# Kernel tuning notes

Hardware: AMD Instinct MI355X
Metric: run time of the kernel (lower is better)

## Reference

```python
import jax, jax.numpy as jnp
import numpy as np

HIDDEN = 768
VOCAB = 32000
HS1 = 128


def setup_inputs() -> dict:
    key = jax.random.key(0)
    k_tk, k_hs, k_w1, k_b1, k_w2, k_b2 = jax.random.split(key, 6)
    B, S = 16, 4096
    tk = jax.random.randint(k_tk, (B, S), 0, VOCAB, dtype=jnp.int64)
    hs0 = jax.random.normal(k_hs, (B, S, HIDDEN), dtype=jnp.float32)
    # lin1: in_features = VOCAB + HIDDEN, out = HS1.  Stored as [in, out]
    # (transpose of torch's [out, in]); rows [0:VOCAB] multiply the one-hot,
    # rows [VOCAB:] multiply hs0, matching cat([one_hot, hs0], -1).
    bound1 = 1.0 / np.sqrt(VOCAB + HIDDEN)
    W1 = jax.random.uniform(k_w1, (VOCAB + HIDDEN, HS1), jnp.float32, -bound1, bound1)
    b1 = jax.random.uniform(k_b1, (HS1,), jnp.float32, -bound1, bound1)
    bound2 = 1.0 / np.sqrt(HS1)
    W2 = jax.random.uniform(k_w2, (HS1, 1), jnp.float32, -bound2, bound2)
    b2 = jax.random.uniform(k_b2, (1,), jnp.float32, -bound2, bound2)
    return {"tk": tk, "hs0": hs0, "W1": W1, "b1": b1, "W2": W2, "b2": b2}


def reference(tk, hs0, W1, b1, W2, b2):
    # one_hot(tk) @ W1[:VOCAB] is exactly a row gather (entries are 0/1),
    # so compute it as a gather fused with the hs0 projection.
    tok_part = W1[:VOCAB][tk]                      # [B, S, HS1] gather
    hs_part = jnp.einsum("bsh,hk->bsk", hs0, W1[VOCAB:])  # [B, S, HS1]
    h = jax.nn.relu(tok_part + hs_part + b1)       # [B, S, HS1]
    out = jnp.einsum("bsk,ko->bso", h, W2) + b2    # [B, S, 1]
    return out.squeeze(-1)                         # [B, S]
```

## Files before the change

### kernel.cpp

```cpp
#include <hip/hip_runtime.h>

#define HIDDEN 768
#define VOCAB  32000
#define HS1    128
#define KSTEPS (HIDDEN / 32)

typedef __attribute__((ext_vector_type(8))) short bf16x8;
typedef __attribute__((ext_vector_type(4))) float f32x4;

__device__ __forceinline__ unsigned short f2bf(float f) {
    union { float f; unsigned u; } x; x.f = f;
    unsigned r = x.u + 0x7fffu + ((x.u >> 16) & 1u);
    return (unsigned short)(r >> 16);
}

__global__ void pack_b_kernel(const float* __restrict__ W1,
                              unsigned short* __restrict__ Bp) {
    int idx  = blockIdx.x * 256 + threadIdx.x;
    int j    = idx & 7;
    int lane = (idx >> 3) & 63;
    int nt   = (idx >> 9) & 7;
    int ks   = idx >> 12;
    int k = ks * 32 + (lane >> 4) * 8 + j;
    int n = nt * 16 + (lane & 15);
    float v = W1[(size_t)(VOCAB + k) * HS1 + n];
    Bp[idx] = f2bf(v);
}

__launch_bounds__(256, 2)
__global__ void classifier_kernel(const int* __restrict__ tk,
                                  const float* __restrict__ hs0,
                                  const float* __restrict__ W1,
                                  const float* __restrict__ b1,
                                  const float* __restrict__ W2,
                                  const float* __restrict__ b2,
                                  const unsigned short* __restrict__ Bp,
                                  float* __restrict__ out) {
    const int lane = threadIdx.x & 63;
    const int wave = threadIdx.x >> 6;
    const int quad = lane >> 4;
    const int col  = lane & 15;
    const int row0 = (blockIdx.x * 4 + wave) * 32;

    const float* pa0 = hs0 + (size_t)(row0 + col) * HIDDEN + quad * 8;
    const float* pa1 = pa0 + (size_t)16 * HIDDEN;
    const unsigned short* pb0 = Bp + lane * 8;

    int toks[8];
#pragma unroll
    for (int mt = 0; mt < 2; ++mt)
#pragma unroll
        for (int reg = 0; reg < 4; ++reg)
            toks[mt * 4 + reg] = tk[row0 + mt * 16 + quad * 4 + reg];

    f32x4 acc[2][8];
#pragma unroll
    for (int mt = 0; mt < 2; ++mt)
#pragma unroll
        for (int nt = 0; nt < 8; ++nt)
            acc[mt][nt] = (f32x4){0.f, 0.f, 0.f, 0.f};

    struct Frag {
        f32x4 a0l, a0h, a1l, a1h;
        bf16x8 b[8];
    };

    auto load_frag = [&](int ks) {
        Frag f;
        const f32x4* x0 = (const f32x4*)(pa0 + ks * 32);
        const f32x4* x1 = (const f32x4*)(pa1 + ks * 32);
        f.a0l = __builtin_nontemporal_load(x0);
        f.a0h = __builtin_nontemporal_load(x0 + 1);
        f.a1l = __builtin_nontemporal_load(x1);
        f.a1h = __builtin_nontemporal_load(x1 + 1);
        const unsigned short* pb  = pb0 + ks * 4096;
        const unsigned short* pb2 = pb + 2048;
#pragma unroll
        for (int nt = 0; nt < 4; ++nt) {
            f.b[nt]     = *(const bf16x8*)(pb  + nt * 512);
            f.b[nt + 4] = *(const bf16x8*)(pb2 + nt * 512);
        }
        return f;
    };

    auto cvt8 = [&](f32x4 lo, f32x4 hi) {
        bf16x8 r;
        r[0] = (short)f2bf(lo[0]); r[1] = (short)f2bf(lo[1]);
        r[2] = (short)f2bf(lo[2]); r[3] = (short)f2bf(lo[3]);
        r[4] = (short)f2bf(hi[0]); r[5] = (short)f2bf(hi[1]);
        r[6] = (short)f2bf(hi[2]); r[7] = (short)f2bf(hi[3]);
        return r;
    };

    auto compute = [&](const Frag& f) {
        bf16x8 af0 = cvt8(f.a0l, f.a0h);
        bf16x8 af1 = cvt8(f.a1l, f.a1h);
#pragma unroll
        for (int nt = 0; nt < 8; ++nt) {
            acc[0][nt] = __builtin_amdgcn_mfma_f32_16x16x32_bf16(af0, f.b[nt], acc[0][nt], 0, 0, 0);
            acc[1][nt] = __builtin_amdgcn_mfma_f32_16x16x32_bf16(af1, f.b[nt], acc[1][nt], 0, 0, 0);
        }
    };

    Frag f0 = load_frag(0);
    Frag f1 = load_frag(1);
    Frag f2 = load_frag(2);
#pragma unroll 1
    for (int ks = 3; ks < KSTEPS; ks += 3) {
        compute(f0); f0 = load_frag(ks);
        compute(f1); f1 = load_frag(ks + 1);
        compute(f2); f2 = load_frag(ks + 2);
    }
    compute(f0);
    compute(f1);
    compute(f2);

    const float bb2 = b2[0];
    float b1v[8], w2v[8];
#pragma unroll
    for (int nt = 0; nt < 8; ++nt) {
        b1v[nt] = b1[nt * 16 + col];
        w2v[nt] = W2[nt * 16 + col];
    }
#pragma unroll
    for (int mt = 0; mt < 2; ++mt) {
#pragma unroll
        for (int reg = 0; reg < 4; ++reg) {
            int r = row0 + mt * 16 + quad * 4 + reg;
            const float* wrow = W1 + (size_t)toks[mt * 4 + reg] * HS1;
            float p = 0.f;
#pragma unroll
            for (int nt = 0; nt < 8; ++nt) {
                float v = acc[mt][nt][reg] + wrow[nt * 16 + col] + b1v[nt];
                v = fmaxf(v, 0.f);
                p = fmaf(v, w2v[nt], p);
            }
            p += __shfl_xor(p, 1);
            p += __shfl_xor(p, 2);
            p += __shfl_xor(p, 4);
            p += __shfl_xor(p, 8);
            if (col == 0) out[r] = p + bb2;
        }
    }
}

extern "C" void kernel_launch(void* const* d_in, const int* in_sizes, int n_in,
                              void* d_out, int out_size, void* d_ws, size_t ws_size,
                              hipStream_t stream) {
    const int*   tk  = (const int*)d_in[0];
    const float* hs0 = (const float*)d_in[1];
    const float* W1  = (const float*)d_in[2];
    const float* b1  = (const float*)d_in[3];
    const float* W2  = (const float*)d_in[4];
    const float* b2  = (const float*)d_in[5];
    float* out = (float*)d_out;
    unsigned short* Bp = (unsigned short*)d_ws;

    pack_b_kernel<<<(HIDDEN * HS1) / 256, 256, 0, stream>>>(W1, Bp);

    int n_tokens = in_sizes[0];
    int grid = n_tokens / 128;
    classifier_kernel<<<grid, 256, 0, stream>>>(tk, hs0, W1, b1, W2, b2, Bp, out);
}
```

Before: 304.4 us.

## Stage hs0 tiles through per-wave LDS with coalesced loads and double buffering

Global reads of hs0 are reorganised so each wave loads full 128-byte row segments (8 lanes per row) into a padded per-wave LDS buffer, then reads MFMA A-fragments from LDS. This replaces the earlier strided per-lane fragment loads, with the aim of better coalescing, and double-buffers LDS with a one-stage register prefetch of global data and B fragments. The pack kernel is also changed to read W1 contiguously and scatter the writes. The risks are added LDS traffic, no explicit barrier (it relies on intra-wave ordering), and a shallower prefetch depth than the previous three-stage register pipeline.

```diff
diff --git a/kernel.cpp b/kernel.cpp
--- a/kernel.cpp
+++ b/kernel.cpp
@@ -3,7 +3,8 @@
 #define HIDDEN 768
 #define VOCAB  32000
 #define HS1    128
-#define KSTEPS (HIDDEN / 32)
+#define NSTAGE 24
+#define LSTRIDE 36
 
 typedef __attribute__((ext_vector_type(8))) short bf16x8;
 typedef __attribute__((ext_vector_type(4))) float f32x4;
@@ -16,15 +17,15 @@
 
 __global__ void pack_b_kernel(const float* __restrict__ W1,
                               unsigned short* __restrict__ Bp) {
-    int idx  = blockIdx.x * 256 + threadIdx.x;
-    int j    = idx & 7;
-    int lane = (idx >> 3) & 63;
-    int nt   = (idx >> 9) & 7;
-    int ks   = idx >> 12;
-    int k = ks * 32 + (lane >> 4) * 8 + j;
-    int n = nt * 16 + (lane & 15);
-    float v = W1[(size_t)(VOCAB + k) * HS1 + n];
-    Bp[idx] = f2bf(v);
+    int tid = blockIdx.x * 256 + threadIdx.x;
+    float v = W1[(size_t)VOCAB * HS1 + tid];
+    int k = tid >> 7;
+    int n = tid & 127;
+    int ks = k >> 5, kr = k & 31;
+    int quad = kr >> 3, j = kr & 7;
+    int nt = n >> 4, c = n & 15;
+    int lane = quad * 16 + c;
+    Bp[(((ks * 8 + nt) * 64 + lane) << 3) + j] = f2bf(v);
 }
 
 __launch_bounds__(256, 2)
@@ -36,15 +37,20 @@
                                   const float* __restrict__ b2,
                                   const unsigned short* __restrict__ Bp,
                                   float* __restrict__ out) {
+    __shared__ float lds[4][2][32 * LSTRIDE];
+
     const int lane = threadIdx.x & 63;
     const int wave = threadIdx.x >> 6;
     const int quad = lane >> 4;
     const int col  = lane & 15;
     const int row0 = (blockIdx.x * 4 + wave) * 32;
 
-    const float* pa0 = hs0 + (size_t)(row0 + col) * HIDDEN + quad * 8;
-    const float* pa1 = pa0 + (size_t)16 * HIDDEN;
-    const unsigned short* pb0 = Bp + lane * 8;
+    float* buf0 = &lds[wave][0][0];
+    float* buf1 = &lds[wave][1][0];
+
+    const int srow = lane >> 3;
+    const int scol = (lane & 7) * 4;
+    const float* gbase = hs0 + (size_t)row0 * HIDDEN;
 
     int toks[8];
 #pragma unroll
@@ -60,27 +66,28 @@
         for (int nt = 0; nt < 8; ++nt)
             acc[mt][nt] = (f32x4){0.f, 0.f, 0.f, 0.f};
 
-    struct Frag {
-        f32x4 a0l, a0h, a1l, a1h;
-        bf16x8 b[8];
+    f32x4 greg[4];
+    auto gload = [&](int s) {
+#pragma unroll
+        for (int i = 0; i < 4; ++i) {
+            const float* p = gbase + (size_t)(i * 8 + srow) * HIDDEN + s * 32 + scol;
+            greg[i] = __builtin_nontemporal_load((const f32x4*)p);
+        }
+    };
+    auto lstore = [&](float* buf) {
+#pragma unroll
+        for (int i = 0; i < 4; ++i)
+            *(f32x4*)(buf + (i * 8 + srow) * LSTRIDE + scol) = greg[i];
     };
 
-    auto load_frag = [&](int ks) {
-        Frag f;
-        const f32x4* x0 = (const f32x4*)(pa0 + ks * 32);
-        const f32x4* x1 = (const f32x4*)(pa1 + ks * 32);
-        f.a0l = __builtin_nontemporal_load(x0);
-        f.a0h = __builtin_nontemporal_load(x0 + 1);
-        f.a1l = __builtin_nontemporal_load(x1);
-        f.a1h = __builtin_nontemporal_load(x1 + 1);
-        const unsigned short* pb  = pb0 + ks * 4096;
-        const unsigned short* pb2 = pb + 2048;
+    const unsigned short* pb0 = Bp + lane * 8;
+    auto loadB = [&](int kstep, bf16x8* b) {
+        const unsigned short* pb = pb0 + kstep * 4096;
 #pragma unroll
         for (int nt = 0; nt < 4; ++nt) {
-            f.b[nt]     = *(const bf16x8*)(pb  + nt * 512);
-            f.b[nt + 4] = *(const bf16x8*)(pb2 + nt * 512);
+            b[nt]     = *(const bf16x8*)(pb + nt * 512);
+            b[nt + 4] = *(const bf16x8*)(pb + 2048 + nt * 512);
         }
-        return f;
     };
 
     auto cvt8 = [&](f32x4 lo, f32x4 hi) {
@@ -92,28 +99,35 @@
         return r;
     };
 
-    auto compute = [&](const Frag& f) {
-        bf16x8 af0 = cvt8(f.a0l, f.a0h);
-        bf16x8 af1 = cvt8(f.a1l, f.a1h);
+    auto stage_body = [&](int s, float* cur, float* alt,
+                          const bf16x8* bc, bf16x8* bn) {
+        if (s + 1 < NSTAGE) loadB(s + 1, bn);
+        if (s + 1 < NSTAGE) lstore(alt);
+        if (s + 2 < NSTAGE) gload(s + 2);
+        const float* p0 = cur + col * LSTRIDE + quad * 8;
+        const float* p1 = p0 + 16 * LSTRIDE;
+        f32x4 a0l = *(const f32x4*)p0, a0h = *(const f32x4*)(p0 + 4);
+        f32x4 a1l = *(const f32x4*)p1, a1h = *(const f32x4*)(p1 + 4);
+        bf16x8 af0 = cvt8(a0l, a0h);
+        bf16x8 af1 = cvt8(a1l, a1h);
 #pragma unroll
         for (int nt = 0; nt < 8; ++nt) {
-            acc[0][nt] = __builtin_amdgcn_mfma_f32_16x16x32_bf16(af0, f.b[nt], acc[0][nt], 0, 0, 0);
-            acc[1][nt] = __builtin_amdgcn_mfma_f32_16x16x32_bf16(af1, f.b[nt], acc[1][nt], 0, 0, 0);
+            acc[0][nt] = __builtin_amdgcn_mfma_f32_16x16x32_bf16(af0, bc[nt], acc[0][nt], 0, 0, 0);
+            acc[1][nt] = __builtin_amdgcn_mfma_f32_16x16x32_bf16(af1, bc[nt], acc[1][nt], 0, 0, 0);
         }
     };
 
-    Frag f0 = load_frag(0);
-    Frag f1 = load_frag(1);
-    Frag f2 = load_frag(2);
+    bf16x8 bfrA[8], bfrB[8];
+    gload(0);
+    lstore(buf0);
+    gload(1);
+    loadB(0, bfrA);
+
 #pragma unroll 1
-    for (int ks = 3; ks < KSTEPS; ks += 3) {
-        compute(f0); f0 = load_frag(ks);
-        compute(f1); f1 = load_frag(ks + 1);
-        compute(f2); f2 = load_frag(ks + 2);
+    for (int s = 0; s < NSTAGE; s += 2) {
+        stage_body(s,     buf0, buf1, bfrA, bfrB);
+        stage_body(s + 1, buf1, buf0, bfrB, bfrA);
     }
-    compute(f0);
-    compute(f1);
-    compute(f2);
 
     const float bb2 = b2[0];
     float b1v[8], w2v[8];
```

Result: faster. 291.8 us (-4.1%).
